# Kernel tuning notes

Hardware: AMD Instinct MI355X
Metric: run time of the kernel (lower is better)

## Reference

```python
import jax, jax.numpy as jnp
import numpy as np

H, D = 8, 64          # num_heads, head_dim
DM = 512              # model/feature dim for q,k,v,pos
B, N, M = 8, 1024, 1024


def relative_shift(x):
    # x: [B, H, N, M] -> Transformer-XL pad/reshape shift trick
    b, h, n, m = x.shape
    x = jnp.pad(x, ((0, 0), (0, 0), (0, 0), (1, 0)))      # [B,H,N,M+1]
    x = x.reshape(b, h, m + 1, n)
    x = x[:, :, 1:, :].reshape(b, h, n, m)
    return x


def setup_inputs() -> dict:
    key = jax.random.key(0)
    ks = jax.random.split(key, 11)
    s = 0.05  # small init scale for numerical stability (glorot-ish)
    return {
        "query": jax.random.normal(ks[0], (B, N, DM), jnp.float32),
        "key": jax.random.normal(ks[1], (B, M, DM), jnp.float32),
        "value": jax.random.normal(ks[2], (B, M, DM), jnp.float32),
        "pos": jax.random.normal(ks[3], (B, M, DM), jnp.float32),
        "query_kernel": jax.random.normal(ks[4], (H, DM, D), jnp.float32) * s,
        "key_kernel": jax.random.normal(ks[5], (H, DM, D), jnp.float32) * s,
        "value_kernel": jax.random.normal(ks[6], (H, DM, D), jnp.float32) * s,
        "pos_kernel": jax.random.normal(ks[7], (H, DM, D), jnp.float32) * s,
        "projection_kernel": jax.random.normal(ks[8], (H, D, DM), jnp.float32) * s,
        "pos_bias_u": jax.random.normal(ks[9], (H, D), jnp.float32) * s,
        "pos_bias_v": jax.random.normal(ks[10], (H, D), jnp.float32) * s,
    }


def reference(query, key, value, pos, query_kernel, key_kernel, value_kernel,
              pos_kernel, projection_kernel, pos_bias_u, pos_bias_v):
    # per-head projections
    q = jnp.einsum("bni,hid->bnhd", query, query_kernel)
    k = jnp.einsum("bmi,hid->bmhd", key, key_kernel)
    v = jnp.einsum("bmi,hid->bmhd", value, value_kernel)
    p = jnp.einsum("bmi,hid->bmhd", pos, pos_kernel)

    q_u = q + pos_bias_u  # broadcast [H,D] over [B,N,H,D]
    q_v = q + pos_bias_v

    logits_u = jnp.einsum("bnhd,bmhd->bhnm", q_u, k)
    logits_v = relative_shift(jnp.einsum("bnhd,bmhd->bhnm", q_v, p))

    m = logits_u.shape[3]
    logits = (logits_u + logits_v[:, :, :, :m]) / jnp.sqrt(
        jnp.asarray(D, logits_u.dtype))

    attn = jax.nn.softmax(logits, axis=-1)            # [B,H,N,M]
    ctx = jnp.einsum("bhnm,bmhd->bnhd", attn, v)      # [B,N,H,D]
    out = jnp.einsum("bnhd,hdo->bno", ctx, projection_kernel)
    return out
```

## Files before the change

kernel.cpp:

```cpp
#include <hip/hip_runtime.h>
#include <hip/hip_bf16.h>
#include <math.h>

#define SB 8
#define SS 1024
#define SDM 512
#define SH 8
#define SD 64

typedef unsigned short ushort;
typedef __attribute__((ext_vector_type(8))) short bf16x8;
typedef __attribute__((ext_vector_type(4))) float f32x4;

#define MFMA16(a, b, c) __builtin_amdgcn_mfma_f32_16x16x32_bf16(a, b, c, 0, 0, 0)

static __device__ __forceinline__ ushort f2b(float f) {
    union { float f; unsigned u; } v; v.f = f;
    unsigned r = v.u + 0x7FFF + ((v.u >> 16) & 1);
    return (ushort)(r >> 16);
}

static __device__ __forceinline__ void gll16(const void* g, void* l) {
    __builtin_amdgcn_global_load_lds(
        (const __attribute__((address_space(1))) unsigned int*)g,
        (__attribute__((address_space(3))) unsigned int*)l, 16, 0, 0);
}

#define XTHREADS 2097152
#define WTHREADS 163840
__global__ __launch_bounds__(256) void convert_kernel(
    const float* __restrict__ q, const float* __restrict__ k,
    const float* __restrict__ v, const float* __restrict__ p,
    const float* __restrict__ qw, const float* __restrict__ kw,
    const float* __restrict__ vw, const float* __restrict__ pw,
    const float* __restrict__ projw,
    ushort* __restrict__ xbf, ushort* __restrict__ wt)
{
    const int gid = blockIdx.x * 256 + threadIdx.x;
    if (gid < XTHREADS) {
        const int which = gid >> 19;
        const float* src = (which == 0) ? q : (which == 1) ? k : (which == 2) ? v : p;
        ushort* dst = xbf + (size_t)which * ((size_t)SB * SS * SDM);
        size_t i = (size_t)(gid & 524287) * 8;
        float4 a = *(const float4*)(src + i);
        float4 b = *(const float4*)(src + i + 4);
        union { ushort u[8]; uint4 v4; } o;
        o.u[0] = f2b(a.x); o.u[1] = f2b(a.y); o.u[2] = f2b(a.z); o.u[3] = f2b(a.w);
        o.u[4] = f2b(b.x); o.u[5] = f2b(b.y); o.u[6] = f2b(b.z); o.u[7] = f2b(b.w);
        *(uint4*)(dst + i) = o.v4;
    } else {
        const int wid = gid - XTHREADS;
        const int which = wid >> 15;
        const int local = wid & 32767;
        const int c  = local >> 6;
        const int k0 = (local & 63) * 8;
        union { ushort u[8]; uint4 v4; } o;
        if (which < 4) {
            const float* W = (which == 0) ? qw : (which == 1) ? kw
                           : (which == 2) ? vw : pw;
            const int h = c >> 6, d = c & 63;
            const float* base = W + (size_t)h * SDM * SD + (size_t)k0 * SD + d;
#pragma unroll
            for (int j = 0; j < 8; ++j) o.u[j] = f2b(base[(size_t)j * SD]);
        } else {
            const float* base = projw + (size_t)k0 * SDM + c;
#pragma unroll
            for (int j = 0; j < 8; ++j) o.u[j] = f2b(base[(size_t)j * SDM]);
        }
        *(uint4*)&wt[(size_t)which * SDM * SDM + (size_t)c * SDM + k0] = o.v4;
    }
}

__global__ __launch_bounds__(256) void projmm_kernel(
    const ushort* __restrict__ xbf, const ushort* __restrict__ wt,
    const float* __restrict__ bias_u, const float* __restrict__ bias_v,
    ushort* __restrict__ quo, ushort* __restrict__ qvo,
    ushort* __restrict__ ko, ushort* __restrict__ po,
    ushort* __restrict__ vto)
{
    __shared__ ushort Asm[128 * 32];
    __shared__ ushort Bsm[128 * 32];
    __shared__ ushort Ct[128][136];

    const int tid  = threadIdx.x;
    const int wave = tid >> 6, lane = tid & 63;
    const int quad = lane >> 4, l15 = lane & 15;
    const int which = blockIdx.z;
    const int row0 = blockIdx.x * 128;
    const int col0 = blockIdx.y * 128;
    const int wr = wave >> 1, wc = wave & 1;

    const ushort* A  = xbf + (size_t)which * ((size_t)SB * SS * SDM) + (size_t)row0 * SDM;
    const ushort* Bw = wt  + (size_t)which * (SDM * SDM) + (size_t)col0 * SDM;

    f32x4 acc[4][4];
#pragma unroll
    for (int i = 0; i < 4; ++i)
#pragma unroll
        for (int j = 0; j < 4; ++j) acc[i][j] = (f32x4){0.f, 0.f, 0.f, 0.f};

    for (int k0 = 0; k0 < SDM; k0 += 32) {
#pragma unroll
        for (int j = 0; j < 2; ++j) {
            int t = j * 256 + tid;
            int r = t >> 2, kp = (t & 3) * 8;
            gll16(A  + (size_t)r * SDM + k0 + kp, (char*)Asm + t * 16);
            gll16(Bw + (size_t)r * SDM + k0 + kp, (char*)Bsm + t * 16);
        }
        __syncthreads();

        bf16x8 af[4], bfr[4];
#pragma unroll
        for (int mt = 0; mt < 4; ++mt)
            af[mt] = *(const bf16x8*)&Asm[(wr * 64 + mt * 16 + l15) * 32 + quad * 8];
#pragma unroll
        for (int nt = 0; nt < 4; ++nt)
            bfr[nt] = *(const bf16x8*)&Bsm[(wc * 64 + nt * 16 + l15) * 32 + quad * 8];
#pragma unroll
        for (int mt = 0; mt < 4; ++mt)
#pragma unroll
            for (int nt = 0; nt < 4; ++nt)
                acc[mt][nt] = MFMA16(af[mt], bfr[nt], acc[mt][nt]);
        __syncthreads();
    }

    const float SC = 0.125f;

    const int strow = tid >> 1;
    const int sthalf = tid & 1;

    if (which == 0) {
#pragma unroll
        for (int nt = 0; nt < 4; ++nt) {
            const int lc = wc * 64 + nt * 16 + l15;
            const float bu = bias_u[col0 + lc];
#pragma unroll
            for (int mt = 0; mt < 4; ++mt) {
                const int lr = wr * 64 + mt * 16 + quad * 4;
#pragma unroll
                for (int r = 0; r < 4; ++r)
                    Ct[lr + r][lc] = f2b((acc[mt][nt][r] + bu) * SC);
            }
        }
        __syncthreads();
        {
            const int R = row0 + strow, b = R >> 10, n = R & 1023;
            const int C = col0 + sthalf * 64, h = C >> 6;
            uint4* dst = (uint4*)(quo + ((size_t)(b * SH + h) * SS + n) * SD);
            const uint4* src = (const uint4*)&Ct[strow][sthalf * 64];
#pragma unroll
            for (int j = 0; j < 8; ++j) dst[j] = src[j];
        }
        __syncthreads();
#pragma unroll
        for (int nt = 0; nt < 4; ++nt) {
            const int lc = wc * 64 + nt * 16 + l15;
            const float bv = bias_v[col0 + lc];
#pragma unroll
            for (int mt = 0; mt < 4; ++mt) {
                const int lr = wr * 64 + mt * 16 + quad * 4;
#pragma unroll
                for (int r = 0; r < 4; ++r)
                    Ct[lr + r][lc] = f2b((acc[mt][nt][r] + bv) * SC);
            }
        }
        __syncthreads();
        {
            const int R = row0 + strow, b = R >> 10, n = R & 1023;
            const int C = col0 + sthalf * 64, h = C >> 6;
            uint4* dst = (uint4*)(qvo + ((size_t)(b * SH + h) * SS + n) * SD);
            const uint4* src = (const uint4*)&Ct[strow][sthalf * 64];
#pragma unroll
            for (int j = 0; j < 8; ++j) dst[j] = src[j];
        }
    } else if (which == 1 || which == 3) {
#pragma unroll
        for (int nt = 0; nt < 4; ++nt) {
            const int lc = wc * 64 + nt * 16 + l15;
#pragma unroll
            for (int mt = 0; mt < 4; ++mt) {
                const int lr = wr * 64 + mt * 16 + quad * 4;
#pragma unroll
                for (int r = 0; r < 4; ++r)
                    Ct[lr + r][lc] = f2b(acc[mt][nt][r]);
            }
        }
        __syncthreads();
        {
            ushort* out = (which == 1) ? ko : po;
            const int R = row0 + strow, b = R >> 10, n = R & 1023;
            const int C = col0 + sthalf * 64, h = C >> 6;
            uint4* dst = (uint4*)(out + ((size_t)(b * SH + h) * SS + n) * SD);
            const uint4* src = (const uint4*)&Ct[strow][sthalf * 64];
#pragma unroll
            for (int j = 0; j < 8; ++j) dst[j] = src[j];
        }
    } else {
#pragma unroll
        for (int nt = 0; nt < 4; ++nt) {
            const int lc = wc * 64 + nt * 16 + l15;
#pragma unroll
            for (int mt = 0; mt < 4; ++mt) {
                const int lr = wr * 64 + mt * 16 + quad * 4;
#pragma unroll
                for (int r = 0; r < 4; ++r)
                    Ct[lc][lr + r] = f2b(acc[mt][nt][r]);
            }
        }
        __syncthreads();
        {
            const int C = col0 + strow, h = C >> 6, d = C & 63;
            const int b = row0 >> 10;
            const int nloc = (row0 & 1023) + sthalf * 64;
            uint4* dst = (uint4*)(vto + (size_t)(b * SH + h) * SS * SD
                                  + ((size_t)((nloc >> 6) * 64 + d)) * 64);
            const uint4* src = (const uint4*)&Ct[strow][sthalf * 64];
#pragma unroll
            for (int j = 0; j < 8; ++j) dst[j] = src[j];
        }
    }
}

static __device__ __forceinline__ bf16x8 sfrag(const ushort* buf, int row, int seg) {
    return *(const bf16x8*)&buf[(size_t)row * 64 + ((seg ^ (row & 7)) * 8)];
}

__global__ __launch_bounds__(256) void attn_kernel(
    const ushort* __restrict__ qu, const ushort* __restrict__ qv,
    const ushort* __restrict__ kk, const ushort* __restrict__ pp,
    const ushort* __restrict__ vt, ushort* __restrict__ ctx)
{
    __shared__ ushort KbBuf[2][64 * 64];
    __shared__ ushort PbBuf[2][128 * 64];
    __shared__ float  Glds[4][16][80];

    const int tid  = threadIdx.x;
    const int wave = tid >> 6;
    const int lane = tid & 63;
    const int quad = lane >> 4;
    const int l15  = lane & 15;

    const int id   = blockIdx.x;
    const int xcd  = id & 7;
    const int slot = id >> 3;
    const int bhid = xcd * 8 + (slot >> 4);
    const int nt   = slot & 15;
    const int b    = bhid >> 3;
    const int h    = bhid & 7;
    const int n0   = nt * 64;

    const size_t bh   = (size_t)(b * SH + h);
    const ushort* qu_bh = qu + bh * SS * SD;
    const ushort* qv_bh = qv + bh * SS * SD;
    const ushort* k_bh  = kk + bh * SS * SD;
    const ushort* p_bh  = pp + bh * SS * SD;
    const ushort* vt_bh = vt + bh * SS * SD;

    const int mcD = n0 >> 6;

    const int arow  = n0 + wave * 16 + l15;
    const int arow2 = (arow + 1 < SS) ? arow + 1 : SS - 1;

    bf16x8 a_u0  = *(const bf16x8*)(qu_bh + (size_t)arow  * SD + quad * 8);
    bf16x8 a_u1  = *(const bf16x8*)(qu_bh + (size_t)arow  * SD + quad * 8 + 32);
    bf16x8 a_vl0 = *(const bf16x8*)(qv_bh + (size_t)arow  * SD + quad * 8);
    bf16x8 a_vl1 = *(const bf16x8*)(qv_bh + (size_t)arow  * SD + quad * 8 + 32);
    bf16x8 a_vu0 = *(const bf16x8*)(qv_bh + (size_t)arow2 * SD + quad * 8);
    bf16x8 a_vu1 = *(const bf16x8*)(qv_bh + (size_t)arow2 * SD + quad * 8 + 32);

    float lsum[4] = {0.f, 0.f, 0.f, 0.f};
    f32x4 O[4];
#pragma unroll
    for (int dt = 0; dt < 4; ++dt) O[dt] = (f32x4){0.f, 0.f, 0.f, 0.f};

    float  (*Gl)[80] = Glds[wave];
    ushort (*Pl)[72] = (ushort (*)[72])Glds[wave];

    auto stage = [&](int mc, int buf) {
        const int m0s = mc * 64;
        const int cb  = (mc <= mcD) ? (m0s - n0 + 960) : (m0s - n0 - 65);
        char* Kd = (char*)KbBuf[buf];
        char* Pd = (char*)PbBuf[buf];
#pragma unroll
        for (int it = 0; it < 2; ++it) {
            int t = it * 256 + tid;
            int r = t >> 3, s = t & 7;
            gll16(k_bh + (size_t)(m0s + r) * 64 + ((s ^ (r & 7)) * 8), Kd + t * 16);
        }
#pragma unroll
        for (int it = 0; it < 4; ++it) {
            int t = it * 256 + tid;
            int r = t >> 3, s = t & 7;
            int c = cb + r; c = (c < 0) ? 0 : (c > SS - 1 ? SS - 1 : c);
            gll16(p_bh + (size_t)c * 64 + ((s ^ (r & 7)) * 8), Pd + t * 16);
        }
    };

    stage(0, 0);

    for (int mc = 0; mc < 16; ++mc) {
        const int m0 = mc * 64;
        const int diff = m0 - n0;
        const bool lowerband = (mc <= mcD);
        const int cur = mc & 1;

        __syncthreads();
        if (mc + 1 < 16) stage(mc + 1, cur ^ 1);

        const ushort* Kc = KbBuf[cur];
        const ushort* Pc = PbBuf[cur];

        bf16x8 vb0[4], vb1[4];
#pragma unroll
        for (int dt = 0; dt < 4; ++dt) {
            const ushort* vp = vt_bh + (size_t)(m0 + dt * 16 + l15) * 64 + quad * 8;
            vb0[dt] = *(const bf16x8*)vp;
            vb1[dt] = *(const bf16x8*)(vp + 32);
        }

        f32x4 S[4];
#pragma unroll
        for (int mt = 0; mt < 4; ++mt) {
            const int r = mt * 16 + l15;
            f32x4 c = (f32x4){0.f, 0.f, 0.f, 0.f};
            c = MFMA16(a_u0, sfrag(Kc, r, quad), c);
            c = MFMA16(a_u1, sfrag(Kc, r, quad + 4), c);
            S[mt] = c;
        }

        float sv[4][4];
#pragma unroll
        for (int mt = 0; mt < 4; ++mt)
#pragma unroll
            for (int r = 0; r < 4; ++r) sv[mt][r] = 0.f;

        {
            const bf16x8 av0 = lowerband ? a_vl0 : a_vu0;
            const bf16x8 av1 = lowerband ? a_vl1 : a_vu1;
#pragma unroll
            for (int ti = 0; ti < 5; ++ti) {
                const int t = (3 - wave + ti) * 16 + l15;
                f32x4 g = (f32x4){0.f, 0.f, 0.f, 0.f};
                g = MFMA16(av0, sfrag(Pc, t, quad), g);
                g = MFMA16(av1, sfrag(Pc, t, quad + 4), g);
#pragma unroll
                for (int r = 0; r < 4; ++r)
                    Gl[quad * 4 + r][ti * 16 + l15] = g[r];
            }
#pragma unroll
            for (int mt = 0; mt < 4; ++mt) {
                const int mloc = mt * 16 + l15;
#pragma unroll
                for (int r = 0; r < 4; ++r) {
                    const int q4r = quad * 4 + r;
                    const int d1 = diff + mloc - (wave * 16 + q4r);
                    const bool use = lowerband ? (d1 <= 0) : (d1 >= 2);
                    if (use) sv[mt][r] = Gl[q4r][mloc - q4r + 15];
                }
            }
        }

        if (mc == mcD) {
            const int cbase = diff - 65;
            bf16x8 pu0[5], pu1[5];
#pragma unroll
            for (int ti = 0; ti < 5; ++ti) {
                int t = (3 - wave + ti) * 16 + l15;
                int c = cbase + t;
                c = (c < 0) ? 0 : (c > SS - 1 ? SS - 1 : c);
                const ushort* pr = p_bh + (size_t)c * SD + quad * 8;
                pu0[ti] = *(const bf16x8*)pr;
                pu1[ti] = *(const bf16x8*)(pr + 32);
            }
#pragma unroll
            for (int ti = 0; ti < 5; ++ti) {
                f32x4 g = (f32x4){0.f, 0.f, 0.f, 0.f};
                g = MFMA16(a_vu0, pu0[ti], g);
                g = MFMA16(a_vu1, pu1[ti], g);
#pragma unroll
                for (int r = 0; r < 4; ++r)
                    Gl[quad * 4 + r][ti * 16 + l15] = g[r];
            }
#pragma unroll
            for (int mt = 0; mt < 4; ++mt) {
                const int mloc = mt * 16 + l15;
#pragma unroll
                for (int r = 0; r < 4; ++r) {
                    const int q4r = quad * 4 + r;
                    const int d1 = diff + mloc - (wave * 16 + q4r);
                    if (d1 >= 2) sv[mt][r] = Gl[q4r][mloc - q4r + 15];
                }
            }
        }

        float e[4][4];
#pragma unroll
        for (int mt = 0; mt < 4; ++mt)
#pragma unroll
            for (int r = 0; r < 4; ++r) {
                e[mt][r] = __expf(S[mt][r] + sv[mt][r]);
                lsum[r] += e[mt][r];
            }

#pragma unroll
        for (int mt = 0; mt < 4; ++mt)
#pragma unroll
            for (int r = 0; r < 4; ++r)
                Pl[quad * 4 + r][mt * 16 + l15] = f2b(e[mt][r]);

        bf16x8 ap0 = *(const bf16x8*)&Pl[l15][quad * 8];
        bf16x8 ap1 = *(const bf16x8*)&Pl[l15][32 + quad * 8];
#pragma unroll
        for (int dt = 0; dt < 4; ++dt) {
            O[dt] = MFMA16(ap0, vb0[dt], O[dt]);
            O[dt] = MFMA16(ap1, vb1[dt], O[dt]);
        }
    }

#pragma unroll
    for (int mask = 1; mask <= 8; mask <<= 1)
#pragma unroll
        for (int r = 0; r < 4; ++r)
            lsum[r] += __shfl_xor(lsum[r], mask, 16);

    float inv[4];
#pragma unroll
    for (int r = 0; r < 4; ++r) inv[r] = 1.f / lsum[r];

#pragma unroll
    for (int dt = 0; dt < 4; ++dt)
#pragma unroll
        for (int r = 0; r < 4; ++r) {
            int nn = n0 + wave * 16 + quad * 4 + r;
            ctx[((size_t)b * SS + nn) * (SH * SD) + h * SD + dt * 16 + l15] =
                f2b(O[dt][r] * inv[r]);
        }
}

__global__ __launch_bounds__(256) void outproj_kernel(
    const ushort* __restrict__ ctx, const ushort* __restrict__ wt,
    float* __restrict__ out)
{
    __shared__ ushort Asm[128 * 32];
    __shared__ ushort Bsm[128 * 32];

    const int tid  = threadIdx.x;
    const int wave = tid >> 6, lane = tid & 63;
    const int quad = lane >> 4, l15 = lane & 15;
    const int row0 = blockIdx.x * 128;
    const int col0 = blockIdx.y * 128;
    const int wr = wave >> 1, wc = wave & 1;

    const ushort* A  = ctx + (size_t)row0 * SDM;
    const ushort* Bw = wt + (size_t)4 * (SDM * SDM) + (size_t)col0 * SDM;

    f32x4 acc[4][4];
#pragma unroll
    for (int i = 0; i < 4; ++i)
#pragma unroll
        for (int j = 0; j < 4; ++j) acc[i][j] = (f32x4){0.f, 0.f, 0.f, 0.f};

    for (int k0 = 0; k0 < SDM; k0 += 32) {
#pragma unroll
        for (int j = 0; j < 2; ++j) {
            int t = j * 256 + tid;
            int r = t >> 2, kp = (t & 3) * 8;
            gll16(A  + (size_t)r * SDM + k0 + kp, (char*)Asm + t * 16);
            gll16(Bw + (size_t)r * SDM + k0 + kp, (char*)Bsm + t * 16);
        }
        __syncthreads();

        bf16x8 af[4], bfr[4];
#pragma unroll
        for (int mt = 0; mt < 4; ++mt)
            af[mt] = *(const bf16x8*)&Asm[(wr * 64 + mt * 16 + l15) * 32 + quad * 8];
#pragma unroll
        for (int nt = 0; nt < 4; ++nt)
            bfr[nt] = *(const bf16x8*)&Bsm[(wc * 64 + nt * 16 + l15) * 32 + quad * 8];
#pragma unroll
        for (int mt = 0; mt < 4; ++mt)
#pragma unroll
            for (int nt = 0; nt < 4; ++nt)
                acc[mt][nt] = MFMA16(af[mt], bfr[nt], acc[mt][nt]);
        __syncthreads();
    }

#pragma unroll
    for (int mt = 0; mt < 4; ++mt)
#pragma unroll
        for (int nt = 0; nt < 4; ++nt) {
            const int R = row0 + wr * 64 + mt * 16 + quad * 4;
            const int C = col0 + wc * 64 + nt * 16 + l15;
#pragma unroll
            for (int r = 0; r < 4; ++r)
                out[(size_t)(R + r) * SDM + C] = acc[mt][nt][r];
        }
}

extern "C" void kernel_launch(void* const* d_in, const int* in_sizes, int n_in,
                              void* d_out, int out_size, void* d_ws, size_t ws_size,
                              hipStream_t stream)
{
    const float* query  = (const float*)d_in[0];
    const float* key    = (const float*)d_in[1];
    const float* value  = (const float*)d_in[2];
    const float* pos    = (const float*)d_in[3];
    const float* qw     = (const float*)d_in[4];
    const float* kw     = (const float*)d_in[5];
    const float* vw     = (const float*)d_in[6];
    const float* pw     = (const float*)d_in[7];
    const float* projw  = (const float*)d_in[8];
    const float* bias_u = (const float*)d_in[9];
    const float* bias_v = (const float*)d_in[10];

    char* w = (char*)d_ws;
    const size_t MB = 1024 * 1024;
    ushort* xbf = (ushort*)w;
    ushort* quo = (ushort*)(w + 32 * MB);
    ushort* qvo = (ushort*)(w + 40 * MB);
    ushort* ko  = (ushort*)(w + 48 * MB);
    ushort* po  = (ushort*)(w + 56 * MB);
    ushort* vto = (ushort*)(w + 64 * MB);
    ushort* wt  = (ushort*)(w + 72 * MB);
    ushort* ctx = (ushort*)w;

    convert_kernel<<<dim3(8832), 256, 0, stream>>>(
        query, key, value, pos, qw, kw, vw, pw, projw, xbf, wt);

    dim3 g1(64, 4, 4);
    projmm_kernel<<<g1, 256, 0, stream>>>(xbf, wt, bias_u, bias_v,
                                          quo, qvo, ko, po, vto);

    attn_kernel<<<dim3(1024), 256, 0, stream>>>(quo, qvo, ko, po, vto, ctx);

    dim3 g3(64, 4);
    outproj_kernel<<<g3, 256, 0, stream>>>(ctx, wt, (float*)d_out);
}
```

Baseline: 279.1 us.

## Fuse input bf16 conversion into projection GEMM and split attention over key halves

Drops the separate fp32-to-bf16 pass over the four activation tensors: the projection GEMM now reads fp32 inputs and converts them while staging the A tile into LDS. The weight conversion gets its own small kernel that transposes through LDS. Attention is split into two key-range halves per query tile with an added combine kernel that sums the bf16 partial outputs and normalises. The attention K/P staging goes from double-buffered to single-buffered, and projmm blocks get an XCD-aware ordering. This removes a large intermediate write and read and doubles attention block count, at the cost of extra partial-output traffic, bf16 rounding of unnormalised partials, and less load/compute overlap in attention.

```diff
diff --git a/kernel.cpp b/kernel.cpp
--- a/kernel.cpp
+++ b/kernel.cpp
@@ -19,6 +19,9 @@
     unsigned r = v.u + 0x7FFF + ((v.u >> 16) & 1);
     return (ushort)(r >> 16);
 }
+static __device__ __forceinline__ float b2f(ushort u) {
+    union { unsigned u; float f; } v; v.u = (unsigned)u << 16; return v.f;
+}
 
 static __device__ __forceinline__ void gll16(const void* g, void* l) {
     __builtin_amdgcn_global_load_lds(
@@ -26,93 +29,119 @@
         (__attribute__((address_space(3))) unsigned int*)l, 16, 0, 0);
 }
 
-#define XTHREADS 2097152
-#define WTHREADS 163840
-__global__ __launch_bounds__(256) void convert_kernel(
-    const float* __restrict__ q, const float* __restrict__ k,
-    const float* __restrict__ v, const float* __restrict__ p,
+__global__ __launch_bounds__(256) void convert_w_kernel(
     const float* __restrict__ qw, const float* __restrict__ kw,
     const float* __restrict__ vw, const float* __restrict__ pw,
-    const float* __restrict__ projw,
-    ushort* __restrict__ xbf, ushort* __restrict__ wt)
+    const float* __restrict__ projw, ushort* __restrict__ wt)
 {
-    const int gid = blockIdx.x * 256 + threadIdx.x;
-    if (gid < XTHREADS) {
-        const int which = gid >> 19;
-        const float* src = (which == 0) ? q : (which == 1) ? k : (which == 2) ? v : p;
-        ushort* dst = xbf + (size_t)which * ((size_t)SB * SS * SDM);
-        size_t i = (size_t)(gid & 524287) * 8;
-        float4 a = *(const float4*)(src + i);
-        float4 b = *(const float4*)(src + i + 4);
-        union { ushort u[8]; uint4 v4; } o;
-        o.u[0] = f2b(a.x); o.u[1] = f2b(a.y); o.u[2] = f2b(a.z); o.u[3] = f2b(a.w);
-        o.u[4] = f2b(b.x); o.u[5] = f2b(b.y); o.u[6] = f2b(b.z); o.u[7] = f2b(b.w);
-        *(uint4*)(dst + i) = o.v4;
+    __shared__ ushort T[64][72];
+    const int id = blockIdx.x;
+    const int tid = threadIdx.x;
+
+    if (id < 256) {
+        const int which = id >> 6, h = (id >> 3) & 7, kt = id & 7;
+        const float* W = (which == 0) ? qw : (which == 1) ? kw
+                       : (which == 2) ? vw : pw;
+        const int kk = tid >> 2, d4 = (tid & 3) * 16;
+        const float* src = W + ((size_t)h * SDM + kt * 64 + kk) * SD + d4;
+#pragma unroll
+        for (int j = 0; j < 4; ++j) {
+            float4 v = *(const float4*)(src + j * 4);
+            T[kk][d4 + j * 4 + 0] = f2b(v.x); T[kk][d4 + j * 4 + 1] = f2b(v.y);
+            T[kk][d4 + j * 4 + 2] = f2b(v.z); T[kk][d4 + j * 4 + 3] = f2b(v.w);
+        }
+        __syncthreads();
+        const int d = tid >> 2, kseg = (tid & 3) * 16;
+        union { ushort u[16]; uint4 v4[2]; } o;
+#pragma unroll
+        for (int j = 0; j < 16; ++j) o.u[j] = T[kseg + j][d];
+        uint4* dst = (uint4*)&wt[((size_t)which * SDM + h * 64 + d) * SDM + kt * 64 + kseg];
+        dst[0] = o.v4[0]; dst[1] = o.v4[1];
     } else {
-        const int wid = gid - XTHREADS;
-        const int which = wid >> 15;
-        const int local = wid & 32767;
-        const int c  = local >> 6;
-        const int k0 = (local & 63) * 8;
-        union { ushort u[8]; uint4 v4; } o;
-        if (which < 4) {
-            const float* W = (which == 0) ? qw : (which == 1) ? kw
-                           : (which == 2) ? vw : pw;
-            const int h = c >> 6, d = c & 63;
-            const float* base = W + (size_t)h * SDM * SD + (size_t)k0 * SD + d;
-#pragma unroll
-            for (int j = 0; j < 8; ++j) o.u[j] = f2b(base[(size_t)j * SD]);
-        } else {
-            const float* base = projw + (size_t)k0 * SDM + c;
-#pragma unroll
-            for (int j = 0; j < 8; ++j) o.u[j] = f2b(base[(size_t)j * SDM]);
-        }
-        *(uint4*)&wt[(size_t)which * SDM * SDM + (size_t)c * SDM + k0] = o.v4;
+        const int id2 = id - 256, kt = id2 >> 3, ct = id2 & 7;
+        const int kk = tid >> 2, c4 = (tid & 3) * 16;
+        const float* src = projw + ((size_t)(kt * 64 + kk)) * SDM + ct * 64 + c4;
+#pragma unroll
+        for (int j = 0; j < 4; ++j) {
+            float4 v = *(const float4*)(src + j * 4);
+            T[kk][c4 + j * 4 + 0] = f2b(v.x); T[kk][c4 + j * 4 + 1] = f2b(v.y);
+            T[kk][c4 + j * 4 + 2] = f2b(v.z); T[kk][c4 + j * 4 + 3] = f2b(v.w);
+        }
+        __syncthreads();
+        const int c = tid >> 2, kseg = (tid & 3) * 16;
+        union { ushort u[16]; uint4 v4[2]; } o;
+#pragma unroll
+        for (int j = 0; j < 16; ++j) o.u[j] = T[kseg + j][c];
+        uint4* dst = (uint4*)&wt[(size_t)4 * SDM * SDM
+                                 + ((size_t)(ct * 64 + c)) * SDM + kt * 64 + kseg];
+        dst[0] = o.v4[0]; dst[1] = o.v4[1];
     }
 }
 
 __global__ __launch_bounds__(256) void projmm_kernel(
-    const ushort* __restrict__ xbf, const ushort* __restrict__ wt,
+    const float* __restrict__ xq, const float* __restrict__ xk,
+    const float* __restrict__ xv, const float* __restrict__ xp,
+    const ushort* __restrict__ wt,
     const float* __restrict__ bias_u, const float* __restrict__ bias_v,
     ushort* __restrict__ quo, ushort* __restrict__ qvo,
     ushort* __restrict__ ko, ushort* __restrict__ po,
     ushort* __restrict__ vto)
 {
-    __shared__ ushort Asm[128 * 32];
+    __shared__ ushort Asm[128 * 40];
     __shared__ ushort Bsm[128 * 32];
     __shared__ ushort Ct[128][136];
 
     const int tid  = threadIdx.x;
     const int wave = tid >> 6, lane = tid & 63;
     const int quad = lane >> 4, l15 = lane & 15;
-    const int which = blockIdx.z;
-    const int row0 = blockIdx.x * 128;
-    const int col0 = blockIdx.y * 128;
+
+    const int id  = blockIdx.x;
+    const int xcd = id & 7;
+    const int s   = id >> 3;
+    const int which = s >> 5;
+    const int s5  = s & 31;
+    const int row0 = (xcd * 8 + (s5 >> 2)) * 128;
+    const int col0 = (s5 & 3) * 128;
     const int wr = wave >> 1, wc = wave & 1;
 
-    const ushort* A  = xbf + (size_t)which * ((size_t)SB * SS * SDM) + (size_t)row0 * SDM;
-    const ushort* Bw = wt  + (size_t)which * (SDM * SDM) + (size_t)col0 * SDM;
+    const float* X = (which == 0) ? xq : (which == 1) ? xk : (which == 2) ? xv : xp;
+    const float* A  = X + (size_t)row0 * SDM;
+    const ushort* Bw = wt + (size_t)which * (SDM * SDM) + (size_t)col0 * SDM;
 
     f32x4 acc[4][4];
 #pragma unroll
     for (int i = 0; i < 4; ++i)
 #pragma unroll
         for (int j = 0; j < 4; ++j) acc[i][j] = (f32x4){0.f, 0.f, 0.f, 0.f};
+
+    const int ar = tid >> 1;
+    const int ah = (tid & 1) * 16;
 
     for (int k0 = 0; k0 < SDM; k0 += 32) {
 #pragma unroll
         for (int j = 0; j < 2; ++j) {
             int t = j * 256 + tid;
             int r = t >> 2, kp = (t & 3) * 8;
-            gll16(A  + (size_t)r * SDM + k0 + kp, (char*)Asm + t * 16);
             gll16(Bw + (size_t)r * SDM + k0 + kp, (char*)Bsm + t * 16);
         }
+        {
+            const float* ap = A + (size_t)ar * SDM + k0 + ah;
+            union { ushort u[16]; uint4 v4[2]; } o;
+#pragma unroll
+            for (int j = 0; j < 4; ++j) {
+                float4 v = *(const float4*)(ap + j * 4);
+                o.u[j * 4 + 0] = f2b(v.x); o.u[j * 4 + 1] = f2b(v.y);
+                o.u[j * 4 + 2] = f2b(v.z); o.u[j * 4 + 3] = f2b(v.w);
+            }
+            uint4* dst = (uint4*)&Asm[ar * 40 + ah];
+            dst[0] = o.v4[0]; dst[1] = o.v4[1];
+        }
         __syncthreads();
 
         bf16x8 af[4], bfr[4];
 #pragma unroll
         for (int mt = 0; mt < 4; ++mt)
-            af[mt] = *(const bf16x8*)&Asm[(wr * 64 + mt * 16 + l15) * 32 + quad * 8];
+            af[mt] = *(const bf16x8*)&Asm[(wr * 64 + mt * 16 + l15) * 40 + quad * 8];
 #pragma unroll
         for (int nt = 0; nt < 4; ++nt)
             bfr[nt] = *(const bf16x8*)&Bsm[(wc * 64 + nt * 16 + l15) * 32 + quad * 8];
@@ -125,7 +154,6 @@
     }
 
     const float SC = 0.125f;
-
     const int strow = tid >> 1;
     const int sthalf = tid & 1;
 
@@ -228,10 +256,12 @@
 __global__ __launch_bounds__(256) void attn_kernel(
     const ushort* __restrict__ qu, const ushort* __restrict__ qv,
     const ushort* __restrict__ kk, const ushort* __restrict__ pp,
-    const ushort* __restrict__ vt, ushort* __restrict__ ctx)
+    const ushort* __restrict__ vt,
+    ushort* __restrict__ Op0, ushort* __restrict__ Op1,
+    float* __restrict__ l0, float* __restrict__ l1)
 {
-    __shared__ ushort KbBuf[2][64 * 64];
-    __shared__ ushort PbBuf[2][128 * 64];
+    __shared__ ushort Kb[64 * 64];
+    __shared__ ushort Pb[128 * 64];
     __shared__ float  Glds[4][16][80];
 
     const int tid  = threadIdx.x;
@@ -243,11 +273,14 @@
     const int id   = blockIdx.x;
     const int xcd  = id & 7;
     const int slot = id >> 3;
-    const int bhid = xcd * 8 + (slot >> 4);
-    const int nt   = slot & 15;
+    const int bhid = xcd * 8 + (slot >> 5);
+    const int r5   = slot & 31;
+    const int half = r5 >> 4;
+    const int nt   = r5 & 15;
     const int b    = bhid >> 3;
     const int h    = bhid & 7;
     const int n0   = nt * 64;
+    const int mc0  = half * 8;
 
     const size_t bh   = (size_t)(b * SH + h);
     const ushort* qu_bh = qu + bh * SS * SD;
@@ -276,39 +309,32 @@
     float  (*Gl)[80] = Glds[wave];
     ushort (*Pl)[72] = (ushort (*)[72])Glds[wave];
 
-    auto stage = [&](int mc, int buf) {
+    auto stage = [&](int mc) {
         const int m0s = mc * 64;
         const int cb  = (mc <= mcD) ? (m0s - n0 + 960) : (m0s - n0 - 65);
-        char* Kd = (char*)KbBuf[buf];
-        char* Pd = (char*)PbBuf[buf];
 #pragma unroll
         for (int it = 0; it < 2; ++it) {
             int t = it * 256 + tid;
             int r = t >> 3, s = t & 7;
-            gll16(k_bh + (size_t)(m0s + r) * 64 + ((s ^ (r & 7)) * 8), Kd + t * 16);
+            gll16(k_bh + (size_t)(m0s + r) * 64 + ((s ^ (r & 7)) * 8), (char*)Kb + t * 16);
         }
 #pragma unroll
         for (int it = 0; it < 4; ++it) {
             int t = it * 256 + tid;
             int r = t >> 3, s = t & 7;
             int c = cb + r; c = (c < 0) ? 0 : (c > SS - 1 ? SS - 1 : c);
-            gll16(p_bh + (size_t)c * 64 + ((s ^ (r & 7)) * 8), Pd + t * 16);
+            gll16(p_bh + (size_t)c * 64 + ((s ^ (r & 7)) * 8), (char*)Pb + t * 16);
         }
     };
 
-    stage(0, 0);
-
-    for (int mc = 0; mc < 16; ++mc) {
+    stage(mc0);
+
+    for (int mc = mc0; mc < mc0 + 8; ++mc) {
         const int m0 = mc * 64;
         const int diff = m0 - n0;
         const bool lowerband = (mc <= mcD);
-        const int cur = mc & 1;
-
-        __syncthreads();
-        if (mc + 1 < 16) stage(mc + 1, cur ^ 1);
-
-        const ushort* Kc = KbBuf[cur];
-        const ushort* Pc = PbBuf[cur];
+
+        __syncthreads();
 
         bf16x8 vb0[4], vb1[4];
 #pragma unroll
@@ -323,8 +349,8 @@
         for (int mt = 0; mt < 4; ++mt) {
             const int r = mt * 16 + l15;
             f32x4 c = (f32x4){0.f, 0.f, 0.f, 0.f};
-            c = MFMA16(a_u0, sfrag(Kc, r, quad), c);
-            c = MFMA16(a_u1, sfrag(Kc, r, quad + 4), c);
+            c = MFMA16(a_u0, sfrag(Kb, r, quad), c);
+            c = MFMA16(a_u1, sfrag(Kb, r, quad + 4), c);
             S[mt] = c;
         }
 
@@ -341,8 +367,8 @@
             for (int ti = 0; ti < 5; ++ti) {
                 const int t = (3 - wave + ti) * 16 + l15;
                 f32x4 g = (f32x4){0.f, 0.f, 0.f, 0.f};
-                g = MFMA16(av0, sfrag(Pc, t, quad), g);
-                g = MFMA16(av1, sfrag(Pc, t, quad + 4), g);
+                g = MFMA16(av0, sfrag(Pb, t, quad), g);
+                g = MFMA16(av1, sfrag(Pb, t, quad + 4), g);
 #pragma unroll
                 for (int r = 0; r < 4; ++r)
                     Gl[quad * 4 + r][ti * 16 + l15] = g[r];
@@ -393,6 +419,9 @@
             }
         }
 
+        __syncthreads();
+        if (mc + 1 < mc0 + 8) stage(mc + 1);
+
         float e[4][4];
 #pragma unroll
         for (int mt = 0; mt < 4; ++mt)
@@ -423,18 +452,44 @@
         for (int r = 0; r < 4; ++r)
             lsum[r] += __shfl_xor(lsum[r], mask, 16);
 
-    float inv[4];
-#pragma unroll
-    for (int r = 0; r < 4; ++r) inv[r] = 1.f / lsum[r];
+    ushort* Op = half ? Op1 : Op0;
+    float*  lp = half ? l1  : l0;
 
 #pragma unroll
     for (int dt = 0; dt < 4; ++dt)
 #pragma unroll
         for (int r = 0; r < 4; ++r) {
             int nn = n0 + wave * 16 + quad * 4 + r;
-            ctx[((size_t)b * SS + nn) * (SH * SD) + h * SD + dt * 16 + l15] =
-                f2b(O[dt][r] * inv[r]);
-        }
+            Op[((size_t)b * SS + nn) * (SH * SD) + h * SD + dt * 16 + l15] =
+                f2b(O[dt][r]);
+        }
+    if (l15 == 0) {
+#pragma unroll
+        for (int r = 0; r < 4; ++r) {
+            int nn = n0 + wave * 16 + quad * 4 + r;
+            lp[((size_t)b * SS + nn) * SH + h] = lsum[r];
+        }
+    }
+}
+
+__global__ __launch_bounds__(256) void combine_kernel(
+    const ushort* __restrict__ Op0, const ushort* __restrict__ Op1,
+    const float* __restrict__ l0, const float* __restrict__ l1,
+    ushort* __restrict__ ctx)
+{
+    const int gid = blockIdx.x * 256 + threadIdx.x;
+    const size_t E = (size_t)gid * 8;
+    const int row = gid >> 6;
+    const int h   = (gid & 63) >> 3;
+    const float inv = 1.f / (l0[(size_t)row * SH + h] + l1[(size_t)row * SH + h]);
+
+    union { ushort u[8]; uint4 v4; } a, bo, o;
+    a.v4  = *(const uint4*)(Op0 + E);
+    bo.v4 = *(const uint4*)(Op1 + E);
+#pragma unroll
+    for (int j = 0; j < 8; ++j)
+        o.u[j] = f2b((b2f(a.u[j]) + b2f(bo.u[j])) * inv);
+    *(uint4*)(ctx + E) = o.v4;
 }
 
 __global__ __launch_bounds__(256) void outproj_kernel(
@@ -515,23 +570,28 @@
 
     char* w = (char*)d_ws;
     const size_t MB = 1024 * 1024;
-    ushort* xbf = (ushort*)w;
-    ushort* quo = (ushort*)(w + 32 * MB);
-    ushort* qvo = (ushort*)(w + 40 * MB);
-    ushort* ko  = (ushort*)(w + 48 * MB);
-    ushort* po  = (ushort*)(w + 56 * MB);
-    ushort* vto = (ushort*)(w + 64 * MB);
-    ushort* wt  = (ushort*)(w + 72 * MB);
-    ushort* ctx = (ushort*)w;
-
-    convert_kernel<<<dim3(8832), 256, 0, stream>>>(
-        query, key, value, pos, qw, kw, vw, pw, projw, xbf, wt);
-
-    dim3 g1(64, 4, 4);
-    projmm_kernel<<<g1, 256, 0, stream>>>(xbf, wt, bias_u, bias_v,
-                                          quo, qvo, ko, po, vto);
-
-    attn_kernel<<<dim3(1024), 256, 0, stream>>>(quo, qvo, ko, po, vto, ctx);
+    ushort* quo = (ushort*)(w);
+    ushort* qvo = (ushort*)(w + 8 * MB);
+    ushort* ko  = (ushort*)(w + 16 * MB);
+    ushort* po  = (ushort*)(w + 24 * MB);
+    ushort* vto = (ushort*)(w + 32 * MB);
+    ushort* wt  = (ushort*)(w + 40 * MB);
+    ushort* ctx = (ushort*)(w + 43 * MB);
+    ushort* Op0 = (ushort*)(w + 51 * MB);
+    ushort* Op1 = (ushort*)(w + 59 * MB);
+    float*  l0  = (float*)(w + 67 * MB);
+    float*  l1  = (float*)(w + 67 * MB + 262144);
+
+    convert_w_kernel<<<dim3(320), 256, 0, stream>>>(qw, kw, vw, pw, projw, wt);
+
+    projmm_kernel<<<dim3(1024), 256, 0, stream>>>(query, key, value, pos, wt,
+                                                  bias_u, bias_v,
+                                                  quo, qvo, ko, po, vto);
+
+    attn_kernel<<<dim3(2048), 256, 0, stream>>>(quo, qvo, ko, po, vto,
+                                                Op0, Op1, l0, l1);
+
+    combine_kernel<<<dim3(2048), 256, 0, stream>>>(Op0, Op1, l0, l1, ctx);
 
     dim3 g3(64, 4);
     outproj_kernel<<<g3, 256, 0, stream>>>(ctx, wt, (float*)d_out);
```

Result: slower. 323.5 us (+15.9%).
